# Kernel tuning notes

Hardware: AMD Instinct MI355X
Metric: run time of the kernel (lower is better)

Reference implementation:

```python
import jax, jax.numpy as jnp
import numpy as np

N = 100000   # nodes
E = 1600000  # edges (avg degree 16)
F = 256      # in_channels
H = 4        # heads
C = 32       # out_channels per head
NEG_SLOPE = 0.2  # PyG GATConv default leaky_relu slope


def setup_inputs() -> dict:
    key = jax.random.key(0)
    k0, k1, k2, k3, k4 = jax.random.split(key, 5)
    x = jax.random.normal(k0, (N, F), dtype=jnp.float32)
    edge_index = jax.random.randint(k1, (2, E), 0, N, dtype=jnp.int32)
    W = jax.random.normal(k2, (F, H * C), dtype=jnp.float32) * 0.05
    att_src = jax.random.normal(k3, (H, C), dtype=jnp.float32) * 0.05
    att_dst = jax.random.normal(k4, (H, C), dtype=jnp.float32) * 0.05
    bias = jnp.zeros((H * C,), dtype=jnp.float32)
    return {"x": x, "edge_index": edge_index, "W": W,
            "att_src": att_src, "att_dst": att_dst, "bias": bias}


def reference(x, edge_index, W, att_src, att_dst, bias):
    n = x.shape[0]
    h_, c_ = att_src.shape
    # add self loops (PyG default add_self_loops=True)
    loops = jnp.arange(n, dtype=edge_index.dtype)
    src = jnp.concatenate([edge_index[0], loops])  # source node j of each edge
    dst = jnp.concatenate([edge_index[1], loops])  # target node i of each edge
    # linear projection, per-head view: [N, H, C]
    h = (x @ W).reshape(n, h_, c_)
    # per-node attention halves: [N, H]
    a_src = jnp.einsum('nhc,hc->nh', h, att_src)
    a_dst = jnp.einsum('nhc,hc->nh', h, att_dst)
    # per-edge logits with leaky relu: [Etot, H]
    e = jax.nn.leaky_relu(a_src[src] + a_dst[dst], NEG_SLOPE)
    # segment softmax over edges sharing the same destination
    m = jax.ops.segment_max(e, dst, num_segments=n)
    m = jnp.where(jnp.isfinite(m), m, jnp.zeros_like(m))  # isolated nodes
    p = jnp.exp(e - m[dst])
    s = jax.ops.segment_sum(p, dst, num_segments=n)
    alpha = p / (s[dst] + 1e-16)  # [Etot, H]
    # weighted scatter-aggregate of source features
    msg = h[src] * alpha[:, :, None]  # [Etot, H, C]
    out = jax.ops.segment_sum(msg, dst, num_segments=n)  # [N, H, C]
    return out.reshape(n, h_ * c_) + bias
```

## Files before the change

kernel.cpp:

```cpp
#include <hip/hip_runtime.h>

#define NEG_SLOPE 0.2f
#define CAP 64
#define NPART 8
#define BUILD_GROUPS 128

typedef __attribute__((ext_vector_type(8))) short short8;
typedef __attribute__((ext_vector_type(4))) float f32x4;

__device__ __forceinline__ float lrelu(float x) {
    return x > 0.0f ? x : NEG_SLOPE * x;
}

__device__ __forceinline__ unsigned short f2bf(float f) {
    unsigned int u = __float_as_uint(f);
    u += 0x7FFFu + ((u >> 16) & 1u);
    return (unsigned short)(u >> 16);
}

__device__ __forceinline__ float2 bfpair(unsigned int u) {
    float2 r;
    r.x = __uint_as_float(u << 16);
    r.y = __uint_as_float(u & 0xFFFF0000u);
    return r;
}

__global__ void convW_kernel(const float* __restrict__ W, unsigned short* __restrict__ Wtf) {
    int idx = blockIdx.x * blockDim.x + threadIdx.x;
    int j = idx & 7;
    int lane = (idx >> 3) & 63;
    int f = idx >> 9;
    int t = f >> 3;
    int ks = f & 7;
    int k = ks * 32 + (lane >> 4) * 8 + j;
    int nn = t * 16 + (lane & 15);
    Wtf[idx] = f2bf(W[k * 128 + nn]);
}

__global__ __launch_bounds__(256) void front_kernel(
    const float* __restrict__ x, const unsigned short* __restrict__ Wtf,
    const float* __restrict__ att_src, const float* __restrict__ att_dst,
    const int* __restrict__ esrc, const int* __restrict__ edst,
    int* __restrict__ deg, int* __restrict__ bucket,
    unsigned short* __restrict__ hb, float* __restrict__ a_src,
    float* __restrict__ a_dst, int n, int e, int gg) {
    int tid = threadIdx.x;
    int g = blockIdx.x >> 3;
    int lg = blockIdx.x & 7;
    bool isGemm;
    int idx;
    if (g < 2 * gg) {
        isGemm = ((g & 1) == 0);
        idx = (g >> 1) * 8 + lg;
    } else {
        isGemm = false;
        idx = gg * 8 + (g - 2 * gg) * 8 + lg;
    }

    if (!isGemm) {
        int p = idx & 7;
        int slice = idx >> 3;
        int part = (n + NPART - 1) / NPART;
        unsigned lo = (unsigned)(p * part);
        int e4 = e >> 2;
        int stride = BUILD_GROUPS * 256;
        const int4* dst4 = (const int4*)edst;
        const int4* src4 = (const int4*)esrc;
        for (int i = slice * 256 + tid; i < e4; i += stride) {
            int4 d4 = dst4[i];
            int4 s4 = src4[i];
            if ((unsigned)(d4.x - lo) < (unsigned)part) {
                int r = atomicAdd(&deg[d4.x], 1);
                if (r < CAP) bucket[d4.x * CAP + r] = s4.x;
            }
            if ((unsigned)(d4.y - lo) < (unsigned)part) {
                int r = atomicAdd(&deg[d4.y], 1);
                if (r < CAP) bucket[d4.y * CAP + r] = s4.y;
            }
            if ((unsigned)(d4.z - lo) < (unsigned)part) {
                int r = atomicAdd(&deg[d4.z], 1);
                if (r < CAP) bucket[d4.z * CAP + r] = s4.z;
            }
            if ((unsigned)(d4.w - lo) < (unsigned)part) {
                int r = atomicAdd(&deg[d4.w], 1);
                if (r < CAP) bucket[d4.w * CAP + r] = s4.w;
            }
        }
        if (idx == 0 && tid < (e & 3)) {
            int i = e4 * 4 + tid;
            int d = edst[i];
            int r = atomicAdd(&deg[d], 1);
            if (r < CAP) bucket[d * CAP + r] = esrc[i];
        }
        return;
    }

    int wave = tid >> 6;
    int lane = tid & 63;
    int ln = lane & 15;
    int quad = lane >> 4;
    int row0w = idx * 128 + wave * 32;

    int r0 = row0w + ln;       if (r0 >= n) r0 = n - 1;
    int r1 = row0w + 16 + ln;  if (r1 >= n) r1 = n - 1;
    const float* xr0 = &x[(size_t)r0 * 256];
    const float* xr1 = &x[(size_t)r1 * 256];

    f32x4 acc[2][8];
    #pragma unroll
    for (int rt = 0; rt < 2; ++rt)
        #pragma unroll
        for (int t = 0; t < 8; ++t) acc[rt][t] = (f32x4){0.f, 0.f, 0.f, 0.f};

    #pragma unroll
    for (int ks = 0; ks < 8; ++ks) {
        int ko = ks * 32 + quad * 8;
        float4 a00 = *(const float4*)&xr0[ko];
        float4 a01 = *(const float4*)&xr0[ko + 4];
        float4 a10 = *(const float4*)&xr1[ko];
        float4 a11 = *(const float4*)&xr1[ko + 4];
        short8 af0, af1;
        af0[0] = (short)f2bf(a00.x); af0[1] = (short)f2bf(a00.y);
        af0[2] = (short)f2bf(a00.z); af0[3] = (short)f2bf(a00.w);
        af0[4] = (short)f2bf(a01.x); af0[5] = (short)f2bf(a01.y);
        af0[6] = (short)f2bf(a01.z); af0[7] = (short)f2bf(a01.w);
        af1[0] = (short)f2bf(a10.x); af1[1] = (short)f2bf(a10.y);
        af1[2] = (short)f2bf(a10.z); af1[3] = (short)f2bf(a10.w);
        af1[4] = (short)f2bf(a11.x); af1[5] = (short)f2bf(a11.y);
        af1[6] = (short)f2bf(a11.z); af1[7] = (short)f2bf(a11.w);
        #pragma unroll
        for (int t = 0; t < 8; ++t) {
            short8 bf = *(const short8*)&Wtf[(size_t)(((t * 8 + ks) * 64) + lane) * 8];
            acc[0][t] = __builtin_amdgcn_mfma_f32_16x16x32_bf16(af0, bf, acc[0][t], 0, 0, 0);
            acc[1][t] = __builtin_amdgcn_mfma_f32_16x16x32_bf16(af1, bf, acc[1][t], 0, 0, 0);
        }
    }

    #pragma unroll
    for (int rt = 0; rt < 2; ++rt) {
        #pragma unroll
        for (int t = 0; t < 8; ++t) {
            #pragma unroll
            for (int r = 0; r < 4; ++r) {
                int grow = row0w + rt * 16 + quad * 4 + r;
                if (grow < n) hb[(size_t)grow * 128 + t * 16 + ln] = f2bf(acc[rt][t][r]);
            }
        }
    }

    #pragma unroll
    for (int hd = 0; hd < 4; ++hd) {
        float as1 = att_src[hd * 32 + ln];
        float as2 = att_src[hd * 32 + 16 + ln];
        float ad1 = att_dst[hd * 32 + ln];
        float ad2 = att_dst[hd * 32 + 16 + ln];
        #pragma unroll
        for (int rt = 0; rt < 2; ++rt) {
            #pragma unroll
            for (int r = 0; r < 4; ++r) {
                float ps = acc[rt][2 * hd][r] * as1 + acc[rt][2 * hd + 1][r] * as2;
                float pd = acc[rt][2 * hd][r] * ad1 + acc[rt][2 * hd + 1][r] * ad2;
                #pragma unroll
                for (int off = 1; off < 16; off <<= 1) {
                    ps += __shfl_xor(ps, off);
                    pd += __shfl_xor(pd, off);
                }
                if (ln == 0) {
                    int grow = row0w + rt * 16 + quad * 4 + r;
                    if (grow < n) {
                        a_src[grow * 4 + hd] = ps;
                        a_dst[grow * 4 + hd] = pd;
                    }
                }
            }
        }
    }
}

__global__ __launch_bounds__(256) void aggregate_kernel(
    const unsigned short* __restrict__ hb, const float* __restrict__ a_src,
    const float* __restrict__ a_dst, const int* __restrict__ deg,
    const int* __restrict__ bucket, const float* __restrict__ bias,
    float* __restrict__ out, int n) {
    __shared__ float lds_alpha[4][CAP][4];
    __shared__ int lds_s[4][CAP];
    int wave = threadIdx.x >> 6;
    int lane = threadIdx.x & 63;
    int node = blockIdx.x * 4 + wave;
    if (node >= n) node = n - 1;
    int el = lane & 15;
    int hh = lane >> 4;

    int cnt = deg[node];
    if (cnt > CAP) cnt = CAP;

    float adst = a_dst[node * 4 + hh];
    float e_self = lrelu(a_src[node * 4 + hh] + adst);

    float e_gp[4];
    int s_gp[4];
    float mloc = e_self;
    #pragma unroll
    for (int g = 0; g < 4; ++g) {
        int p = g * 16 + el;
        if (p < cnt) {
            int s = bucket[(unsigned)node * CAP + p];
            s_gp[g] = s;
            float ev = lrelu(a_src[s * 4 + hh] + adst);
            e_gp[g] = ev;
            mloc = fmaxf(mloc, ev);
        } else {
            s_gp[g] = node;
            e_gp[g] = -INFINITY;
        }
    }
    #pragma unroll
    for (int off = 1; off < 16; off <<= 1)
        mloc = fmaxf(mloc, __shfl_xor(mloc, off));

    float pe_gp[4];
    float dloc = 0.0f;
    #pragma unroll
    for (int g = 0; g < 4; ++g) {
        float pe = __expf(e_gp[g] - mloc);
        pe_gp[g] = pe;
        dloc += pe;
    }
    #pragma unroll
    for (int off = 1; off < 16; off <<= 1)
        dloc += __shfl_xor(dloc, off);

    float pe_self = __expf(e_self - mloc);
    float inv = 1.0f / (dloc + pe_self);
    float alpha_self = pe_self * inv;

    #pragma unroll
    for (int g = 0; g < 4; ++g) {
        lds_alpha[wave][g * 16 + el][hh] = pe_gp[g] * inv;
        if (hh == 0) lds_s[wave][g * 16 + el] = s_gp[g];
    }
    __syncthreads();

    const unsigned int* hbu = (const unsigned int*)hb;
    float2 acc;
    {
        float2 hv = bfpair(hbu[(unsigned)node * 64u + lane]);
        acc.x = alpha_self * hv.x;
        acc.y = alpha_self * hv.y;
    }
    int p = 0;
    for (; p + 8 <= cnt; p += 8) {
        int4 sA = *(const int4*)&lds_s[wave][p];
        int4 sB = *(const int4*)&lds_s[wave][p + 4];
        unsigned int v0 = hbu[(unsigned)sA.x * 64u + lane];
        unsigned int v1 = hbu[(unsigned)sA.y * 64u + lane];
        unsigned int v2 = hbu[(unsigned)sA.z * 64u + lane];
        unsigned int v3 = hbu[(unsigned)sA.w * 64u + lane];
        unsigned int v4 = hbu[(unsigned)sB.x * 64u + lane];
        unsigned int v5 = hbu[(unsigned)sB.y * 64u + lane];
        unsigned int v6 = hbu[(unsigned)sB.z * 64u + lane];
        unsigned int v7 = hbu[(unsigned)sB.w * 64u + lane];
        float al0 = lds_alpha[wave][p + 0][hh];
        float al1 = lds_alpha[wave][p + 1][hh];
        float al2 = lds_alpha[wave][p + 2][hh];
        float al3 = lds_alpha[wave][p + 3][hh];
        float al4 = lds_alpha[wave][p + 4][hh];
        float al5 = lds_alpha[wave][p + 5][hh];
        float al6 = lds_alpha[wave][p + 6][hh];
        float al7 = lds_alpha[wave][p + 7][hh];
        float2 h0 = bfpair(v0), h1 = bfpair(v1), h2 = bfpair(v2), h3 = bfpair(v3);
        float2 h4 = bfpair(v4), h5 = bfpair(v5), h6 = bfpair(v6), h7 = bfpair(v7);
        acc.x += al0 * h0.x + al1 * h1.x + al2 * h2.x + al3 * h3.x
               + al4 * h4.x + al5 * h5.x + al6 * h6.x + al7 * h7.x;
        acc.y += al0 * h0.y + al1 * h1.y + al2 * h2.y + al3 * h3.y
               + al4 * h4.y + al5 * h5.y + al6 * h6.y + al7 * h7.y;
    }
    for (; p + 4 <= cnt; p += 4) {
        int4 sA = *(const int4*)&lds_s[wave][p];
        unsigned int v0 = hbu[(unsigned)sA.x * 64u + lane];
        unsigned int v1 = hbu[(unsigned)sA.y * 64u + lane];
        unsigned int v2 = hbu[(unsigned)sA.z * 64u + lane];
        unsigned int v3 = hbu[(unsigned)sA.w * 64u + lane];
        float al0 = lds_alpha[wave][p + 0][hh];
        float al1 = lds_alpha[wave][p + 1][hh];
        float al2 = lds_alpha[wave][p + 2][hh];
        float al3 = lds_alpha[wave][p + 3][hh];
        float2 h0 = bfpair(v0), h1 = bfpair(v1), h2 = bfpair(v2), h3 = bfpair(v3);
        acc.x += al0 * h0.x + al1 * h1.x + al2 * h2.x + al3 * h3.x;
        acc.y += al0 * h0.y + al1 * h1.y + al2 * h2.y + al3 * h3.y;
    }
    for (; p < cnt; ++p) {
        int s = lds_s[wave][p];
        float al = lds_alpha[wave][p][hh];
        float2 hv = bfpair(hbu[(unsigned)s * 64u + lane]);
        acc.x += al * hv.x;
        acc.y += al * hv.y;
    }

    int oc = hh * 32 + el * 2;
    float2 b2 = *(const float2*)&bias[oc];
    float2 o;
    o.x = acc.x + b2.x;
    o.y = acc.y + b2.y;
    *(float2*)&out[(size_t)node * 128 + oc] = o;
}

extern "C" void kernel_launch(void* const* d_in, const int* in_sizes, int n_in,
                              void* d_out, int out_size, void* d_ws, size_t ws_size,
                              hipStream_t stream) {
    const float* x = (const float*)d_in[0];
    const int* edge_index = (const int*)d_in[1];
    const float* W = (const float*)d_in[2];
    const float* att_src = (const float*)d_in[3];
    const float* att_dst = (const float*)d_in[4];
    const float* bias = (const float*)d_in[5];
    float* out = (float*)d_out;

    int n = in_sizes[0] / 256;
    int e = in_sizes[1] / 2;
    const int* esrc = edge_index;
    const int* edst = edge_index + e;

    char* w = (char*)d_ws;
    unsigned short* hb = (unsigned short*)w;  w += (size_t)n * 128 * 2;
    float* a_src = (float*)w;                 w += (size_t)n * 4 * 4;
    float* a_dst = (float*)w;                 w += (size_t)n * 4 * 4;
    unsigned short* Wtf = (unsigned short*)w; w += 128 * 256 * 2;
    int* deg = (int*)w;                       w += (size_t)n * 4;
    int* bucket = (int*)w;                    w += (size_t)n * CAP * 4;

    hipMemsetAsync(deg, 0, (size_t)n * sizeof(int), stream);

    convW_kernel<<<128, 256, 0, stream>>>(W, Wtf);

    int ngb = (n + 127) / 128;
    int gg = (ngb + 7) / 8;
    int grid = (gg + BUILD_GROUPS) * 8;
    front_kernel<<<grid, 256, 0, stream>>>(x, Wtf, att_src, att_dst, esrc, edst,
                                           deg, bucket, hb, a_src, a_dst,
                                           n, e, gg);
    aggregate_kernel<<<(n + 3) / 4, 256, 0, stream>>>(hb, a_src, a_dst, deg,
                                                      bucket, bias, out, n);
}
```

Measured before the change: 374.5 us.

## Stage W tiles in LDS, use packed bf16 converts, fold deg memset into convW

The GEMM path now stages each quarter of the pre-swizzled bf16 W into shared memory once per block, so the waves read B fragments from LDS instead of each reloading them from global memory. The x-to-bf16 and output conversions use the hardware packed v_cvt_pk_bf16_f32 instruction, and hb stores become 32-bit pairs assembled through a lane shuffle. The separate hipMemsetAsync of deg is removed and the zeroing is folded into convW_kernel, saving one launch. In exchange the kernel adds block barriers and 16KB of LDS, which may lower occupancy for the co-scheduled bucket-building blocks. Rounding of the packed convert may also differ slightly from the manual rounding it replaces.

```diff
diff --git a/kernel.cpp b/kernel.cpp
--- a/kernel.cpp
+++ b/kernel.cpp
@@ -7,6 +7,7 @@
 
 typedef __attribute__((ext_vector_type(8))) short short8;
 typedef __attribute__((ext_vector_type(4))) float f32x4;
+typedef __attribute__((ext_vector_type(4))) unsigned int u32x4;
 
 __device__ __forceinline__ float lrelu(float x) {
     return x > 0.0f ? x : NEG_SLOPE * x;
@@ -16,6 +17,12 @@
     unsigned int u = __float_as_uint(f);
     u += 0x7FFFu + ((u >> 16) & 1u);
     return (unsigned short)(u >> 16);
+}
+
+__device__ __forceinline__ unsigned int cvtpk(float lo, float hi) {
+    unsigned int r;
+    asm("v_cvt_pk_bf16_f32 %0, %1, %2" : "=v"(r) : "v"(lo), "v"(hi));
+    return r;
 }
 
 __device__ __forceinline__ float2 bfpair(unsigned int u) {
@@ -25,7 +32,8 @@
     return r;
 }
 
-__global__ void convW_kernel(const float* __restrict__ W, unsigned short* __restrict__ Wtf) {
+__global__ void convW_kernel(const float* __restrict__ W, unsigned short* __restrict__ Wtf,
+                             int* __restrict__ deg, int n) {
     int idx = blockIdx.x * blockDim.x + threadIdx.x;
     int j = idx & 7;
     int lane = (idx >> 3) & 63;
@@ -35,6 +43,7 @@
     int k = ks * 32 + (lane >> 4) * 8 + j;
     int nn = t * 16 + (lane & 15);
     Wtf[idx] = f2bf(W[k * 128 + nn]);
+    for (int z = idx; z < n; z += 32768) deg[z] = 0;
 }
 
 __global__ __launch_bounds__(256) void front_kernel(
@@ -44,6 +53,7 @@
     int* __restrict__ deg, int* __restrict__ bucket,
     unsigned short* __restrict__ hb, float* __restrict__ a_src,
     float* __restrict__ a_dst, int n, int e, int gg) {
+    __shared__ unsigned short Bs[8192];
     int tid = threadIdx.x;
     int g = blockIdx.x >> 3;
     int lg = blockIdx.x & 7;
@@ -113,37 +123,60 @@
         for (int t = 0; t < 8; ++t) acc[rt][t] = (f32x4){0.f, 0.f, 0.f, 0.f};
 
     #pragma unroll
-    for (int ks = 0; ks < 8; ++ks) {
-        int ko = ks * 32 + quad * 8;
-        float4 a00 = *(const float4*)&xr0[ko];
-        float4 a01 = *(const float4*)&xr0[ko + 4];
-        float4 a10 = *(const float4*)&xr1[ko];
-        float4 a11 = *(const float4*)&xr1[ko + 4];
-        short8 af0, af1;
-        af0[0] = (short)f2bf(a00.x); af0[1] = (short)f2bf(a00.y);
-        af0[2] = (short)f2bf(a00.z); af0[3] = (short)f2bf(a00.w);
-        af0[4] = (short)f2bf(a01.x); af0[5] = (short)f2bf(a01.y);
-        af0[6] = (short)f2bf(a01.z); af0[7] = (short)f2bf(a01.w);
-        af1[0] = (short)f2bf(a10.x); af1[1] = (short)f2bf(a10.y);
-        af1[2] = (short)f2bf(a10.z); af1[3] = (short)f2bf(a10.w);
-        af1[4] = (short)f2bf(a11.x); af1[5] = (short)f2bf(a11.y);
-        af1[6] = (short)f2bf(a11.z); af1[7] = (short)f2bf(a11.w);
-        #pragma unroll
-        for (int t = 0; t < 8; ++t) {
-            short8 bf = *(const short8*)&Wtf[(size_t)(((t * 8 + ks) * 64) + lane) * 8];
-            acc[0][t] = __builtin_amdgcn_mfma_f32_16x16x32_bf16(af0, bf, acc[0][t], 0, 0, 0);
-            acc[1][t] = __builtin_amdgcn_mfma_f32_16x16x32_bf16(af1, bf, acc[1][t], 0, 0, 0);
-        }
-    }
-
+    for (int q = 0; q < 4; ++q) {
+        if (q) __syncthreads();
+        #pragma unroll
+        for (int it = 0; it < 4; ++it) {
+            int gi = it * 256 + tid;
+            int t = gi >> 7;
+            int r = gi & 127;
+            *(short8*)&Bs[t * 1024 + r * 8] =
+                *(const short8*)&Wtf[t * 4096 + q * 1024 + r * 8];
+        }
+        __syncthreads();
+
+        #pragma unroll
+        for (int kk = 0; kk < 2; ++kk) {
+            int ks = q * 2 + kk;
+            int ko = ks * 32 + quad * 8;
+            float4 a00 = *(const float4*)&xr0[ko];
+            float4 a01 = *(const float4*)&xr0[ko + 4];
+            float4 a10 = *(const float4*)&xr1[ko];
+            float4 a11 = *(const float4*)&xr1[ko + 4];
+            u32x4 u0, u1;
+            u0.x = cvtpk(a00.x, a00.y);
+            u0.y = cvtpk(a00.z, a00.w);
+            u0.z = cvtpk(a01.x, a01.y);
+            u0.w = cvtpk(a01.z, a01.w);
+            u1.x = cvtpk(a10.x, a10.y);
+            u1.y = cvtpk(a10.z, a10.w);
+            u1.z = cvtpk(a11.x, a11.y);
+            u1.w = cvtpk(a11.z, a11.w);
+            short8 af0 = __builtin_bit_cast(short8, u0);
+            short8 af1 = __builtin_bit_cast(short8, u1);
+            #pragma unroll
+            for (int t = 0; t < 8; ++t) {
+                short8 bf = *(const short8*)&Bs[t * 1024 + kk * 512 + lane * 8];
+                acc[0][t] = __builtin_amdgcn_mfma_f32_16x16x32_bf16(af0, bf, acc[0][t], 0, 0, 0);
+                acc[1][t] = __builtin_amdgcn_mfma_f32_16x16x32_bf16(af1, bf, acc[1][t], 0, 0, 0);
+            }
+        }
+    }
+
+    bool evenln = (ln & 1) == 0;
     #pragma unroll
     for (int rt = 0; rt < 2; ++rt) {
         #pragma unroll
         for (int t = 0; t < 8; ++t) {
             #pragma unroll
             for (int r = 0; r < 4; ++r) {
+                float v = acc[rt][t][r];
+                float vn = __shfl_down(v, 1);
                 int grow = row0w + rt * 16 + quad * 4 + r;
-                if (grow < n) hb[(size_t)grow * 128 + t * 16 + ln] = f2bf(acc[rt][t][r]);
+                if (evenln && grow < n) {
+                    unsigned int pk = cvtpk(v, vn);
+                    *(unsigned int*)&hb[(size_t)grow * 128 + t * 16 + ln] = pk;
+                }
             }
         }
     }
@@ -329,9 +362,7 @@
     int* deg = (int*)w;                       w += (size_t)n * 4;
     int* bucket = (int*)w;                    w += (size_t)n * CAP * 4;
 
-    hipMemsetAsync(deg, 0, (size_t)n * sizeof(int), stream);
-
-    convW_kernel<<<128, 256, 0, stream>>>(W, Wtf);
+    convW_kernel<<<128, 256, 0, stream>>>(W, Wtf, deg, n);
 
     int ngb = (n + 127) / 128;
     int gg = (ngb + 7) / 8;
```

Result: no change. 368.0 us (-1.7%).
